# Optimization experiments

Hardware: AMD Instinct MI355X
Metric: run time of the kernel (lower is better)

Reference implementation:

```python
import jax, jax.numpy as jnp
import numpy as np

N_NODES = 50000


def setup_inputs() -> dict:
    key = jax.random.key(0)
    k1, k2, k3, k4, k5 = jax.random.split(key, 5)
    x = jax.random.normal(k1, (N_NODES, 256), dtype=jnp.float32)
    edge_row = jax.random.randint(k2, (800000,), 0, N_NODES, dtype=jnp.int32)
    edge_col = jax.random.randint(k3, (800000,), 0, N_NODES, dtype=jnp.int32)
    edge_val = jax.random.uniform(k4, (800000,), dtype=jnp.float32)
    W = jax.random.normal(k5, (256, 256), dtype=jnp.float32) * 0.0625  # ~1/sqrt(256)
    b = jnp.zeros((256,), dtype=jnp.float32)
    return {"x": x, "edge_row": edge_row, "edge_col": edge_col,
            "edge_val": edge_val, "W": W, "b": b}


def reference(x, edge_row, edge_col, edge_val, W, b):
    # SpMM: agg[i] = sum_{e: row(e)=i} val(e) * x[col(e)]
    msgs = edge_val[:, None] * x[edge_col]                      # [E, F_in]
    agg = jax.ops.segment_sum(msgs, edge_row, num_segments=N_NODES)  # [N, F_in]
    # nn.Linear: agg @ W.T + b
    return jnp.einsum('nf,of->no', agg, W) + b
```

## Files before the change

### kernel.cpp

```cpp
#include <hip/hip_runtime.h>

typedef unsigned short u16;
typedef __attribute__((ext_vector_type(8))) short short8;
typedef __attribute__((ext_vector_type(4))) float f32x4;
typedef __attribute__((ext_vector_type(4))) u16 u16x4;

#define F 256

__device__ __forceinline__ u16 f2bf(float f) {
  unsigned u = __float_as_uint(f);
  unsigned r = u + 0x7fffu + ((u >> 16) & 1u);
  return (u16)(r >> 16);
}

__device__ __forceinline__ f32x4 bf4_to_f32(u16x4 u) {
  f32x4 x;
#pragma unroll
  for (int j = 0; j < 4; j++) x[j] = __uint_as_float((unsigned)u[j] << 16);
  return x;
}

__device__ __forceinline__ void gemm_body(const float* __restrict__ x,
                                          const float* __restrict__ Wm,
                                          u16* __restrict__ yb,
                                          int NT, int gidx, int stride) {
  int w = (int)(threadIdx.x >> 6);
  int lane = threadIdx.x & 63;
  int ln = lane & 15, q = lane >> 4;

  short8 Bf[4][8];
#pragma unroll
  for (int j = 0; j < 4; j++) {
#pragma unroll
    for (int t = 0; t < 8; t++) {
      const f32x4* wp = (const f32x4*)(Wm + (size_t)((4 * w + j) * 16 + ln) * F + t * 32 + q * 8);
      f32x4 wlo = wp[0], whi = wp[1];
      short8 bfrag;
#pragma unroll
      for (int i = 0; i < 4; i++) {
        bfrag[i]     = (short)f2bf(wlo[i]);
        bfrag[4 + i] = (short)f2bf(whi[i]);
      }
      Bf[j][t] = bfrag;
    }
  }

  for (int mt = gidx; mt < NT; mt += stride) {
    const float* arow = x + (size_t)(mt * 16 + ln) * F + q * 8;
    f32x4 acc[4];
#pragma unroll
    for (int j = 0; j < 4; j++) acc[j] = (f32x4){0.f, 0.f, 0.f, 0.f};

#pragma unroll
    for (int t = 0; t < 8; t++) {
      const f32x4* a4 = (const f32x4*)(arow + t * 32);
      f32x4 alo = a4[0], ahi = a4[1];
      short8 a;
#pragma unroll
      for (int j = 0; j < 4; j++) {
        a[j]     = (short)f2bf(alo[j]);
        a[4 + j] = (short)f2bf(ahi[j]);
      }
#pragma unroll
      for (int j = 0; j < 4; j++) {
        acc[j] = __builtin_amdgcn_mfma_f32_16x16x32_bf16(a, Bf[j][t], acc[j], 0, 0, 0);
      }
    }

    int m0 = mt * 16;
#pragma unroll
    for (int j = 0; j < 4; j++) {
#pragma unroll
      for (int r = 0; r < 4; r++) {
        yb[(size_t)(m0 + q * 4 + r) * F + (4 * w + j) * 16 + ln] = f2bf(acc[j][r]);
      }
    }
  }
}

__global__ void __launch_bounds__(256, 2) fused_k(const float* __restrict__ x,
                                                  const float* __restrict__ Wm,
                                                  u16* __restrict__ yb, int NT, int nGemm,
                                                  const int* __restrict__ erow,
                                                  const int* __restrict__ ecol,
                                                  const float* __restrict__ eval,
                                                  int* __restrict__ curp,
                                                  int2* __restrict__ epk,
                                                  int E, int nScat, int CAP) {
  int bid = blockIdx.x;
  if (bid % 7 == 0) {
    int gidx = bid / 7;
    if (gidx < nGemm) gemm_body(x, Wm, yb, NT, gidx, nGemm);
  } else {
    int sidx = bid - bid / 7 - 1;
    for (int e = sidx * 256 + (int)threadIdx.x; e < E; e += nScat * 256) {
      int r = erow[e];
      int p = atomicAdd(&curp[r << 4], 1);
      if (p < CAP) epk[(size_t)r * CAP + p] = make_int2(ecol[e], __float_as_int(eval[e]));
    }
  }
}

__global__ void __launch_bounds__(256) gather_dir_k(const int* __restrict__ curp,
                                                    const int2* __restrict__ epk,
                                                    const u16* __restrict__ yb,
                                                    const float* __restrict__ bias,
                                                    float* __restrict__ out, int NN, int CAP) {
  int wave = (int)((blockIdx.x * 256 + threadIdx.x) >> 6);
  int lane = threadIdx.x & 63;
  if (wave >= NN) return;
  int deg = curp[wave << 4];
  if (deg > CAP) deg = CAP;
  int s = wave * CAP, e = s + deg;

  f32x4 acc0 = ((const f32x4*)bias)[lane];
  f32x4 acc1 = (f32x4){0.f, 0.f, 0.f, 0.f};
  f32x4 acc2 = (f32x4){0.f, 0.f, 0.f, 0.f};
  f32x4 acc3 = (f32x4){0.f, 0.f, 0.f, 0.f};

  int k = s;
  for (; k + 4 <= e; k += 4) {
    int2 p0 = epk[k], p1 = epk[k + 1], p2 = epk[k + 2], p3 = epk[k + 3];
    u16x4 u0 = *(const u16x4*)(yb + (size_t)p0.x * F + lane * 4);
    u16x4 u1 = *(const u16x4*)(yb + (size_t)p1.x * F + lane * 4);
    u16x4 u2 = *(const u16x4*)(yb + (size_t)p2.x * F + lane * 4);
    u16x4 u3 = *(const u16x4*)(yb + (size_t)p3.x * F + lane * 4);
    acc0 += __int_as_float(p0.y) * bf4_to_f32(u0);
    acc1 += __int_as_float(p1.y) * bf4_to_f32(u1);
    acc2 += __int_as_float(p2.y) * bf4_to_f32(u2);
    acc3 += __int_as_float(p3.y) * bf4_to_f32(u3);
  }
  for (; k < e; k++) {
    int2 p = epk[k];
    u16x4 u = *(const u16x4*)(yb + (size_t)p.x * F + lane * 4);
    acc0 += __int_as_float(p.y) * bf4_to_f32(u);
  }
  acc0 += acc1;
  acc2 += acc3;
  acc0 += acc2;
  ((f32x4*)out)[(size_t)wave * 64 + lane] = acc0;
}


__global__ void hist_k(const int* __restrict__ erow, int* __restrict__ off, int E) {
  int e = blockIdx.x * 256 + threadIdx.x;
  if (e < E) atomicAdd(&off[erow[e] + 1], 1);
}

__global__ void scanA_k(int* __restrict__ a, int* __restrict__ blks, int n) {
  __shared__ int s[256];
  int t = threadIdx.x;
  int i = blockIdx.x * 256 + t;
  s[t] = (i < n) ? a[i] : 0;
  __syncthreads();
  for (int d = 1; d < 256; d <<= 1) {
    int v = (t >= d) ? s[t - d] : 0;
    __syncthreads();
    s[t] += v;
    __syncthreads();
  }
  if (i < n) a[i] = s[t];
  if (t == 255) blks[blockIdx.x] = s[255];
}

__global__ void scanB_k(int* __restrict__ a, const int* __restrict__ blks,
                        int* __restrict__ cur, int n, int nn, int nb) {
  __shared__ int s[256];
  int t = threadIdx.x;
  s[t] = (t < nb) ? blks[t] : 0;
  __syncthreads();
  for (int d = 1; d < 256; d <<= 1) {
    int v = (t >= d) ? s[t - d] : 0;
    __syncthreads();
    s[t] += v;
    __syncthreads();
  }
  int prefix = (blockIdx.x == 0) ? 0 : s[blockIdx.x - 1];
  int i = blockIdx.x * 256 + t;
  if (i < n) {
    int v = a[i] + prefix;
    a[i] = v;
    if (i < nn) cur[i] = v;
  }
}

__global__ void scatter_csr_k(const int* __restrict__ erow, const int* __restrict__ ecol,
                              const float* __restrict__ eval, int* __restrict__ cur,
                              int2* __restrict__ epk, int E) {
  int e = blockIdx.x * 256 + threadIdx.x;
  if (e < E) {
    int r = erow[e];
    int p = atomicAdd(&cur[r], 1);
    epk[p] = make_int2(ecol[e], __float_as_int(eval[e]));
  }
}

__global__ void __launch_bounds__(256, 2) gemm_only_k(const float* __restrict__ x,
                                                      const float* __restrict__ Wm,
                                                      u16* __restrict__ yb, int NT, int stride) {
  gemm_body(x, Wm, yb, NT, blockIdx.x, stride);
}

__global__ void __launch_bounds__(256) gather_csr_k(const int* __restrict__ off,
                                                    const int2* __restrict__ epk,
                                                    const u16* __restrict__ yb,
                                                    const float* __restrict__ bias,
                                                    float* __restrict__ out, int NN) {
  int wave = (int)((blockIdx.x * 256 + threadIdx.x) >> 6);
  int lane = threadIdx.x & 63;
  if (wave >= NN) return;
  int s = off[wave], e = off[wave + 1];

  f32x4 acc0 = ((const f32x4*)bias)[lane];
  f32x4 acc1 = (f32x4){0.f, 0.f, 0.f, 0.f};
  f32x4 acc2 = (f32x4){0.f, 0.f, 0.f, 0.f};
  f32x4 acc3 = (f32x4){0.f, 0.f, 0.f, 0.f};

  int k = s;
  for (; k + 4 <= e; k += 4) {
    int2 p0 = epk[k], p1 = epk[k + 1], p2 = epk[k + 2], p3 = epk[k + 3];
    u16x4 u0 = *(const u16x4*)(yb + (size_t)p0.x * F + lane * 4);
    u16x4 u1 = *(const u16x4*)(yb + (size_t)p1.x * F + lane * 4);
    u16x4 u2 = *(const u16x4*)(yb + (size_t)p2.x * F + lane * 4);
    u16x4 u3 = *(const u16x4*)(yb + (size_t)p3.x * F + lane * 4);
    acc0 += __int_as_float(p0.y) * bf4_to_f32(u0);
    acc1 += __int_as_float(p1.y) * bf4_to_f32(u1);
    acc2 += __int_as_float(p2.y) * bf4_to_f32(u2);
    acc3 += __int_as_float(p3.y) * bf4_to_f32(u3);
  }
  for (; k < e; k++) {
    int2 p = epk[k];
    u16x4 u = *(const u16x4*)(yb + (size_t)p.x * F + lane * 4);
    acc0 += __int_as_float(p.y) * bf4_to_f32(u);
  }
  acc0 += acc1;
  acc2 += acc3;
  acc0 += acc2;
  ((f32x4*)out)[(size_t)wave * 64 + lane] = acc0;
}

extern "C" void kernel_launch(void* const* d_in, const int* in_sizes, int n_in,
                              void* d_out, int out_size, void* d_ws, size_t ws_size,
                              hipStream_t stream) {
  const float* x    = (const float*)d_in[0];
  const int*   erow = (const int*)d_in[1];
  const int*   ecol = (const int*)d_in[2];
  const float* eval = (const float*)d_in[3];
  const float* Wm   = (const float*)d_in[4];
  const float* bias = (const float*)d_in[5];
  float* out = (float*)d_out;

  int NN = in_sizes[0] / F;
  int E  = in_sizes[1];

  char* base = (char*)d_ws;
  size_t o = 0;
  auto carve = [&](size_t bytes) {
    void* p = base + o;
    o += (bytes + 255) & ~(size_t)255;
    return p;
  };
  u16* yb   = (u16*)carve((size_t)NN * F * 2);
  int* curp = (int*)carve((size_t)NN * 64);

  size_t avail = (ws_size > o) ? (ws_size - o) : 0;
  size_t capmax = avail / ((size_t)NN * 8);
  int CAP = (capmax >= 64) ? 64 : (int)capmax;

  int NT = (NN + 15) / 16;

  if (CAP >= 48) {
    int2* epk = (int2*)carve((size_t)NN * CAP * 8);
    hipMemsetAsync(curp, 0, (size_t)NN * 64, stream);
    int G = 3640;
    int nGemm = (G + 6) / 7;
    int nScat = G - nGemm;
    fused_k<<<G, 256, 0, stream>>>(x, Wm, yb, NT, nGemm,
                                   erow, ecol, eval, curp, epk, E, nScat, CAP);
    gather_dir_k<<<(NN + 3) / 4, 256, 0, stream>>>(curp, epk, yb, bias, out, NN, CAP);
  } else {
    int*  cur  = curp;
    int*  off  = (int*)carve((size_t)(NN + 1) * 4);
    int*  blks = (int*)carve(256 * 4);
    int2* epk  = (int2*)carve((size_t)E * 8);
    int nOff = NN + 1;
    int nbOff = (nOff + 255) / 256;
    int nbE = (E + 255) / 256;
    hipMemsetAsync(off, 0, (size_t)nOff * 4, stream);
    hist_k<<<nbE, 256, 0, stream>>>(erow, off, E);
    scanA_k<<<nbOff, 256, 0, stream>>>(off, blks, nOff);
    scanB_k<<<nbOff, 256, 0, stream>>>(off, blks, cur, nOff, NN, nbOff);
    scatter_csr_k<<<nbE, 256, 0, stream>>>(erow, ecol, eval, cur, epk, E);
    gemm_only_k<<<512, 256, 0, stream>>>(x, Wm, yb, NT, 512);
    gather_csr_k<<<(NN + 3) / 4, 256, 0, stream>>>(off, epk, yb, bias, out, NN);
  }
}
```

Measured before the change: 263.9 us.

## Split fused GEMM/scatter kernel and fold counter zeroing into GEMM kernel

Replaces the single heterogeneous kernel, which interleaved GEMM blocks with edge-scatter blocks, with a GEMM kernel that also zeroes the per-row counters, followed by a separate one-edge-per-thread scatter kernel. This removes the hipMemsetAsync launch and makes GEMM and scatter run back to back instead of concurrently. It also changes GEMM launch bounds to one block per SM. The cost is giving up the overlap of the compute-bound GEMM with the atomic-heavy scatter.

```diff
diff --git a/kernel.cpp b/kernel.cpp
--- a/kernel.cpp
+++ b/kernel.cpp
@@ -78,26 +78,26 @@
   }
 }
 
-__global__ void __launch_bounds__(256, 2) fused_k(const float* __restrict__ x,
-                                                  const float* __restrict__ Wm,
-                                                  u16* __restrict__ yb, int NT, int nGemm,
-                                                  const int* __restrict__ erow,
-                                                  const int* __restrict__ ecol,
-                                                  const float* __restrict__ eval,
-                                                  int* __restrict__ curp,
-                                                  int2* __restrict__ epk,
-                                                  int E, int nScat, int CAP) {
-  int bid = blockIdx.x;
-  if (bid % 7 == 0) {
-    int gidx = bid / 7;
-    if (gidx < nGemm) gemm_body(x, Wm, yb, NT, gidx, nGemm);
-  } else {
-    int sidx = bid - bid / 7 - 1;
-    for (int e = sidx * 256 + (int)threadIdx.x; e < E; e += nScat * 256) {
-      int r = erow[e];
-      int p = atomicAdd(&curp[r << 4], 1);
-      if (p < CAP) epk[(size_t)r * CAP + p] = make_int2(ecol[e], __float_as_int(eval[e]));
-    }
+__global__ void __launch_bounds__(256, 1) gemmzero_k(const float* __restrict__ x,
+                                                     const float* __restrict__ Wm,
+                                                     u16* __restrict__ yb,
+                                                     int NT, int stride,
+                                                     int4* __restrict__ zp, int zeroN4) {
+  int tid = blockIdx.x * 256 + (int)threadIdx.x;
+  for (int i = tid; i < zeroN4; i += stride * 256) zp[i] = make_int4(0, 0, 0, 0);
+  gemm_body(x, Wm, yb, NT, blockIdx.x, stride);
+}
+
+__global__ void __launch_bounds__(256) scatter_k(const int* __restrict__ erow,
+                                                 const int* __restrict__ ecol,
+                                                 const float* __restrict__ eval,
+                                                 int* __restrict__ curp,
+                                                 int2* __restrict__ epk, int E, int CAP) {
+  int e = blockIdx.x * 256 + (int)threadIdx.x;
+  if (e < E) {
+    int r = erow[e];
+    int p = atomicAdd(&curp[r << 4], 1);
+    if (p < CAP) epk[(size_t)r * CAP + p] = make_int2(ecol[e], __float_as_int(eval[e]));
   }
 }
 
@@ -195,12 +195,6 @@
   }
 }
 
-__global__ void __launch_bounds__(256, 2) gemm_only_k(const float* __restrict__ x,
-                                                      const float* __restrict__ Wm,
-                                                      u16* __restrict__ yb, int NT, int stride) {
-  gemm_body(x, Wm, yb, NT, blockIdx.x, stride);
-}
-
 __global__ void __launch_bounds__(256) gather_csr_k(const int* __restrict__ off,
                                                     const int2* __restrict__ epk,
                                                     const u16* __restrict__ yb,
@@ -239,6 +233,12 @@
   ((f32x4*)out)[(size_t)wave * 64 + lane] = acc0;
 }
 
+__global__ void __launch_bounds__(256, 1) gemm_only_k(const float* __restrict__ x,
+                                                      const float* __restrict__ Wm,
+                                                      u16* __restrict__ yb, int NT, int stride) {
+  gemm_body(x, Wm, yb, NT, blockIdx.x, stride);
+}
+
 extern "C" void kernel_launch(void* const* d_in, const int* in_sizes, int n_in,
                               void* d_out, int out_size, void* d_ws, size_t ws_size,
                               hipStream_t stream) {
@@ -271,12 +271,10 @@
 
   if (CAP >= 48) {
     int2* epk = (int2*)carve((size_t)NN * CAP * 8);
-    hipMemsetAsync(curp, 0, (size_t)NN * 64, stream);
-    int G = 3640;
-    int nGemm = (G + 6) / 7;
-    int nScat = G - nGemm;
-    fused_k<<<G, 256, 0, stream>>>(x, Wm, yb, NT, nGemm,
-                                   erow, ecol, eval, curp, epk, E, nScat, CAP);
+    int nBlocks = 512;
+    int zeroN4 = NN * 16 / 4;
+    gemmzero_k<<<nBlocks, 256, 0, stream>>>(x, Wm, yb, NT, nBlocks, (int4*)curp, zeroN4);
+    scatter_k<<<(E + 255) / 256, 256, 0, stream>>>(erow, ecol, eval, curp, epk, E, CAP);
     gather_dir_k<<<(NN + 3) / 4, 256, 0, stream>>>(curp, epk, yb, bias, out, NN, CAP);
   } else {
     int*  cur  = curp;
```

Measured after the change: 240.2 us. 9.0% less time.
